# Optimization experiments

Hardware: AMD Instinct MI355X
Metric: run time of the kernel (lower is better)

The kernel has to match this reference:

```python
import jax, jax.numpy as jnp
import numpy as np

B, C, H, W = 8, 256, 32, 32
DK, HEADS = 64, 4
DQ = DK * HEADS            # lambda attention: query dim = dim_key * num_heads
DV = 256 // HEADS          # out_channels // num_heads
EPS = 1e-5
SF = DK ** (-0.25)


def setup_inputs() -> dict:
    key = jax.random.key(0)
    ks = jax.random.split(key, 6)
    inv = 1.0 / np.sqrt(C)
    return {
        "input": jax.random.normal(ks[0], (B, C, H, W), jnp.float32),
        "Wq": jax.random.normal(ks[1], (DQ, C), jnp.float32) * inv,
        "gamma_q": jnp.ones((DQ,), jnp.float32),
        "beta_q": jnp.zeros((DQ,), jnp.float32),
        "Wk": jax.random.normal(ks[2], (DK, C), jnp.float32) * inv,
        "gamma_k": jnp.ones((DK,), jnp.float32),
        "beta_k": jnp.zeros((DK,), jnp.float32),
        "Wv": jax.random.normal(ks[3], (DV, C), jnp.float32) * inv,
        "rpe": jax.random.normal(ks[4], (2 * max(H, W) - 1, 2 * max(H, W) - 1, DK), jnp.float32),
    }


def _bn(x, gamma, beta):
    # BatchNorm2d in training mode: batch stats over (B, H, W), biased variance
    mu = jnp.mean(x, axis=(0, 2, 3), keepdims=True)
    var = jnp.var(x, axis=(0, 2, 3), keepdims=True)
    xn = (x - mu) * jax.lax.rsqrt(var + EPS)
    return xn * gamma[None, :, None, None] + beta[None, :, None, None]


def reference(input, Wq, gamma_q, beta_q, Wk, gamma_k, beta_k, Wv, rpe):
    b, c, h, w = input.shape
    n = h * w
    size = max(h, w)

    # conv1x1 projections (no bias)
    q = _bn(jnp.einsum('oc,bchw->bohw', Wq, input), gamma_q, beta_q)
    k = _bn(jnp.einsum('oc,bchw->bohw', Wk, input), gamma_k, beta_k)
    v = jnp.einsum('oc,bchw->bohw', Wv, input)

    q = q.reshape(b, HEADS, DK, n) * SF          # [b,h,k,n]
    k = k.reshape(b, DK, n) * SF                 # single kv head -> [b,k,n]
    v = v.reshape(b, DV, n)                      # [b,v,n]

    # lambda attention: content lambda
    ks = jax.nn.softmax(k, axis=-1)
    context = jnp.einsum('bkn,bvn->bkv', ks, v)
    out = jnp.einsum('bkv,bhkn->bhvn', context, q)

    # positional lambda via relative position embedding gather
    pos = jnp.arange(size)
    grid = jnp.stack(jnp.meshgrid(pos, pos, indexing='ij'), axis=-1).reshape(-1, 2)  # [n,2]
    rel = grid[None, :] - grid[:, None] + (size - 1)                                 # [n,n,2]
    rg = rpe[rel[..., 0], rel[..., 1]]                                               # [n,n,k]
    pos_context = jnp.einsum('nmk,bvm->bnkv', rg, v)
    out = out + jnp.einsum('bhkn,bnkv->bhvn', q, pos_context)

    return out.reshape(b, -1, h, w)
```

## Files before the change

kernel.cpp:

```cpp
#include <hip/hip_runtime.h>

#define SFC 0.35355339059327373f

typedef __attribute__((ext_vector_type(8))) short short8;
typedef __attribute__((ext_vector_type(16))) float f32x16;
typedef unsigned short ushort_t;

__device__ __forceinline__ float4 ld4(const float* p) { return *reinterpret_cast<const float4*>(p); }
__device__ __forceinline__ void st4(float* p, float4 v) { *reinterpret_cast<float4*>(p) = v; }

union F4 { float4 v; float f[4]; };
union S8 { short8 v; ushort_t u[8]; };

__device__ __forceinline__ ushort_t bfb(float f) {
  union { float f; unsigned u; } a; a.f = f;
  unsigned r = a.u + 0x7FFFu + ((a.u >> 16) & 1u);
  return (ushort_t)(r >> 16);
}
__device__ __forceinline__ float bf2f(ushort_t u) {
  union { unsigned u; float f; } a; a.u = (unsigned)u << 16; return a.f;
}

__device__ __forceinline__ void gl16(const void* g, void* l) {
  __builtin_amdgcn_global_load_lds(
      (const __attribute__((address_space(1))) unsigned int*)g,
      (__attribute__((address_space(3))) unsigned int*)l, 16, 0, 0);
}

__global__ __launch_bounds__(256) void k_prep(
    const float* __restrict__ rpe, const float* __restrict__ wq,
    const float* __restrict__ wk, const float* __restrict__ wv,
    const float* __restrict__ x, ushort_t* __restrict__ RPEB2,
    ushort_t* __restrict__ WB, ushort_t* __restrict__ XBT)
{
  const int bx = blockIdx.x, t = threadIdx.x;
  if (bx < 63) {
    const int di = bx;
#pragma unroll
    for (int it = 0; it < 2; ++it) {
      const int slot = t + it * 256;
      const int tkc = slot >> 6;
      const int l = slot & 63, lnp = l & 31, hip = l >> 5;
      const int dj = (tkc >> 2) * 32 + lnp;
      const int k = (tkc & 3) * 16 + hip * 8;
      S8 o;
      if (dj < 63) {
        const float* s = rpe + (size_t)di * 4032 + dj * 64 + k;
        float4 a = ld4(s), b = ld4(s + 4);
        o.u[0] = bfb(a.x); o.u[1] = bfb(a.y); o.u[2] = bfb(a.z); o.u[3] = bfb(a.w);
        o.u[4] = bfb(b.x); o.u[5] = bfb(b.y); o.u[6] = bfb(b.z); o.u[7] = bfb(b.w);
      } else {
#pragma unroll
        for (int i = 0; i < 8; ++i) o.u[i] = 0;
      }
      *(short8*)(RPEB2 + (size_t)di * 4096 + tkc * 512 + l * 8) = o.v;
    }
  } else if (bx < 111) {
    const int cc = (bx - 63) * 256 + t;
    const int o = cc >> 5, k8 = (cc & 31) * 8;
    const float* src = (o < 256) ? (wq + o * 256)
                      : (o < 320) ? (wk + (o - 256) * 256)
                                  : (wv + (o - 320) * 256);
    float4 a = ld4(src + k8), b = ld4(src + k8 + 4);
    S8 s;
    s.u[0] = bfb(a.x); s.u[1] = bfb(a.y); s.u[2] = bfb(a.z); s.u[3] = bfb(a.w);
    s.u[4] = bfb(b.x); s.u[5] = bfb(b.y); s.u[6] = bfb(b.z); s.u[7] = bfb(b.w);
    *(short8*)(WB + (size_t)o * 256 + k8) = s.v;
  } else {
    const int id = (bx - 111) * 256 + t;
    const int ng = id & 8191, c8 = id >> 13;
    const int bb = ng >> 10, nn = ng & 1023;
    const float* src = x + (size_t)bb * 262144 + (size_t)(c8 * 8) * 1024 + nn;
    S8 s;
#pragma unroll
    for (int j = 0; j < 8; ++j) s.u[j] = bfb(src[(size_t)j * 1024]);
    *(short8*)(XBT + (size_t)ng * 256 + c8 * 8) = s.v;
  }
}

__global__ __launch_bounds__(256) void k_projm(
    const ushort_t* __restrict__ WB, const ushort_t* __restrict__ XBT,
    float* __restrict__ Pk, ushort_t* __restrict__ QB,
    ushort_t* __restrict__ VB2, float* __restrict__ PSUM,
    float* __restrict__ PSQ)
{
  __shared__ ushort_t At[64 * 72];
  __shared__ ushort_t Bt[128 * 72];
  const int t = threadIdx.x;
  const int bm = blockIdx.x, bn = blockIdx.y;
  const int o0 = bm * 64, col0 = bn * 128;
  const int w = t >> 6, l = t & 63, ln = l & 31, hi = l >> 5;
  const int wm = w & 1, wn = w >> 1;

  f32x16 acc0, acc1;
#pragma unroll
  for (int i = 0; i < 16; ++i) { acc0[i] = 0.f; acc1[i] = 0.f; }

  for (int k0 = 0; k0 < 256; k0 += 64) {
    __syncthreads();
#pragma unroll
    for (int i = 0; i < 2; ++i) {
      const int c = t + i * 256, row = c >> 3, k8 = (c & 7) * 8;
      *(short8*)(At + row * 72 + k8) =
          *(const short8*)(WB + (size_t)(o0 + row) * 256 + k0 + k8);
    }
#pragma unroll
    for (int i = 0; i < 4; ++i) {
      const int c = t + i * 256, row = c >> 3, k8 = (c & 7) * 8;
      *(short8*)(Bt + row * 72 + k8) =
          *(const short8*)(XBT + (size_t)(col0 + row) * 256 + k0 + k8);
    }
    __syncthreads();
    const ushort_t* ka  = At + (wm * 32 + ln) * 72 + hi * 8;
    const ushort_t* kb0 = Bt + (wn * 64 + ln) * 72 + hi * 8;
    const ushort_t* kb1 = Bt + (wn * 64 + 32 + ln) * 72 + hi * 8;
#pragma unroll
    for (int kc = 0; kc < 4; ++kc) {
      short8 a = *(const short8*)(ka + kc * 16);
      acc0 = __builtin_amdgcn_mfma_f32_32x32x16_bf16(a, *(const short8*)(kb0 + kc * 16), acc0, 0, 0, 0);
      acc1 = __builtin_amdgcn_mfma_f32_32x32x16_bf16(a, *(const short8*)(kb1 + kc * 16), acc1, 0, 0, 0);
    }
  }

  if (bm == 5) {
    const int b2 = bn >> 3;
    const int n0 = (bn & 7) * 128 + wn * 64 + ln;
#pragma unroll
    for (int r = 0; r < 16; ++r) {
      const int v = wm * 32 + (r & 3) + 8 * (r >> 2) + 4 * hi;
#pragma unroll
      for (int half = 0; half < 2; ++half) {
        const int n = n0 + half * 32;
        const int i2 = n >> 5, j2 = n & 31;
        const float val = half ? acc1[r] : acc0[r];
        VB2[(((size_t)(b2 * 32 + i2) * 2 + wm) * 2 + (j2 >> 4)) * 512
            + ((v & 31) + 32 * ((j2 >> 3) & 1)) * 8 + (j2 & 7)] = bfb(val);
      }
    }
  } else {
    if (bm == 4) {
#pragma unroll
      for (int r = 0; r < 16; ++r) {
        const int o = o0 + wm * 32 + (r & 3) + 8 * (r >> 2) + 4 * hi;
        float* dst = Pk + (size_t)(o - 256) * 8192 + col0 + wn * 64 + ln;
        dst[0]  = acc0[r];
        dst[32] = acc1[r];
      }
    } else {
      const int kcq = 2 * wm;
#pragma unroll
      for (int r = 0; r < 16; ++r) {
        const int kc = kcq + ((r >> 3) & 1);
        const int lq = ln + 32 * ((r >> 2) & 1);
        const int iq = (r & 3) + 4 * hi;
#pragma unroll
        for (int half = 0; half < 2; ++half) {
          const int n = col0 + wn * 64 + half * 32 + ln;
          const int bq_ = n >> 10, i1q = (n >> 5) & 31;
          const float val = half ? acc1[r] : acc0[r];
          QB[(((size_t)(bq_ * 32 + i1q) * 4 + bm) * 4 + kc) * 512 + lq * 8 + iq] =
              bfb(val);
        }
      }
    }
#pragma unroll
    for (int r = 0; r < 16; ++r) {
      float s1 = acc0[r] + acc1[r];
      float s2 = acc0[r] * acc0[r] + acc1[r] * acc1[r];
#pragma unroll
      for (int off = 1; off < 32; off <<= 1) {
        s1 += __shfl_xor(s1, off, 64);
        s2 += __shfl_xor(s2, off, 64);
      }
      if (ln == 0) {
        const int o = o0 + wm * 32 + (r & 3) + 8 * (r >> 2) + 4 * hi;
        PSUM[o * 128 + bn * 2 + wn] = s1;
        PSQ [o * 128 + bn * 2 + wn] = s2;
      }
    }
  }
}

__global__ __launch_bounds__(256) void k_softmax(
    const float* __restrict__ Pk, const float* __restrict__ PSUM,
    const float* __restrict__ PSQ, const float* __restrict__ gq,
    const float* __restrict__ bq, const float* __restrict__ gk,
    const float* __restrict__ bk, float* __restrict__ SCALE,
    float* __restrict__ SHIFT, ushort_t* __restrict__ KSB)
{
  __shared__ float red[8];
  __shared__ float scsh[2];
  const int t = threadIdx.x;

  if (blockIdx.x >= 512) {
    const int ch = blockIdx.x - 512;
    float s1 = 0.f, s2 = 0.f;
    if (t < 128) { s1 = PSUM[ch * 128 + t]; s2 = PSQ[ch * 128 + t]; }
#pragma unroll
    for (int off = 1; off < 64; off <<= 1) {
      s1 += __shfl_xor(s1, off, 64);
      s2 += __shfl_xor(s2, off, 64);
    }
    if ((t & 63) == 0) { red[t >> 6] = s1; red[4 + (t >> 6)] = s2; }
    __syncthreads();
    if (t == 0) {
      s1 = red[0] + red[1] + red[2] + red[3];
      s2 = red[4] + red[5] + red[6] + red[7];
      const float mu = s1 * (1.0f / 8192.0f);
      const float var = s2 * (1.0f / 8192.0f) - mu * mu;
      const float sc = rsqrtf(var + 1e-5f) * gq[ch] * SFC;
      SCALE[ch] = sc;
      SHIFT[ch] = bq[ch] * SFC - mu * sc;
    }
    return;
  }

  const int b = blockIdx.x >> 6, kc = blockIdx.x & 63;
  {
    const int ch = 256 + kc;
    float s1 = 0.f, s2 = 0.f;
    if (t < 128) { s1 = PSUM[ch * 128 + t]; s2 = PSQ[ch * 128 + t]; }
#pragma unroll
    for (int off = 1; off < 64; off <<= 1) {
      s1 += __shfl_xor(s1, off, 64);
      s2 += __shfl_xor(s2, off, 64);
    }
    if ((t & 63) == 0) { red[t >> 6] = s1; red[4 + (t >> 6)] = s2; }
    __syncthreads();
    if (t == 0) {
      s1 = red[0] + red[1] + red[2] + red[3];
      s2 = red[4] + red[5] + red[6] + red[7];
      const float mu = s1 * (1.0f / 8192.0f);
      const float var = s2 * (1.0f / 8192.0f) - mu * mu;
      const float sc = rsqrtf(var + 1e-5f) * gk[kc] * SFC;
      scsh[0] = sc;
      scsh[1] = bk[kc] * SFC - mu * sc;
    }
    __syncthreads();
  }
  const float sc = scsh[0], sh = scsh[1];

  const float4* row = (const float4*)(Pk + (size_t)kc * 8192 + b * 1024);
  float4 v = row[t];
  float y0 = v.x * sc + sh, y1 = v.y * sc + sh;
  float y2 = v.z * sc + sh, y3 = v.w * sc + sh;
  float m = fmaxf(fmaxf(y0, y1), fmaxf(y2, y3));
#pragma unroll
  for (int off = 32; off; off >>= 1) m = fmaxf(m, __shfl_xor(m, off, 64));
  __shared__ float red2[8];
  const int w = t >> 6, lane = t & 63;
  if (lane == 0) red2[w] = m;
  __syncthreads();
  m = fmaxf(fmaxf(red2[0], red2[1]), fmaxf(red2[2], red2[3]));
  const float e0 = __expf(y0 - m), e1 = __expf(y1 - m);
  const float e2 = __expf(y2 - m), e3 = __expf(y3 - m);
  float su = e0 + e1 + e2 + e3;
#pragma unroll
  for (int off = 32; off; off >>= 1) su += __shfl_xor(su, off, 64);
  if (lane == 0) red2[4 + w] = su;
  __syncthreads();
  const float inv = 1.0f / (red2[4] + red2[5] + red2[6] + red2[7]);
  ushort4 u;
  u.x = bfb(e0 * inv); u.y = bfb(e1 * inv);
  u.z = bfb(e2 * inv); u.w = bfb(e3 * inv);
  ((ushort4*)(KSB + (size_t)(b * 64 + kc) * 1024))[t] = u;
}

__global__ __launch_bounds__(256) void k_ctxm(
    const ushort_t* __restrict__ KSB, const ushort_t* __restrict__ VB2,
    ushort_t* __restrict__ CTXB)
{
  __shared__ ushort_t KT[2][64 * 72];
  const int b = blockIdx.x, t = threadIdx.x;
  const int w = t >> 6, l = t & 63, ln = l & 31, hi = l >> 5;
  const int a = w & 1, bt = w >> 1;

  auto stageK = [&](int ch, int buf) {
    const int n0 = ch * 64;
#pragma unroll
    for (int it = 0; it < 2; ++it) {
      const int idx = t + it * 256;
      const int row = idx >> 3, seg = idx & 7;
      *(short8*)(&KT[buf][row * 72 + seg * 8]) =
          *(const short8*)(KSB + (size_t)(b * 64 + row) * 1024 + n0 + seg * 8);
    }
  };

  f32x16 acc;
#pragma unroll
  for (int i = 0; i < 16; ++i) acc[i] = 0.f;

  stageK(0, 0);
  for (int ch = 0; ch < 16; ++ch) {
    const int cur = ch & 1;
    __syncthreads();
    if (ch + 1 < 16) stageK(ch + 1, cur ^ 1);
    const ushort_t* ka = &KT[cur][(a * 32 + ln) * 72 + hi * 8];
#pragma unroll
    for (int cc = 0; cc < 4; ++cc) {
      const int i2 = ch * 2 + (cc >> 1), c = cc & 1;
      short8 bf = *(const short8*)(VB2 +
          (((size_t)(b * 32 + i2) * 2 + bt) * 2 + c) * 512 + l * 8);
      acc = __builtin_amdgcn_mfma_f32_32x32x16_bf16(
          *(const short8*)(ka + cc * 16), bf, acc, 0, 0, 0);
    }
  }
#pragma unroll
  for (int r = 0; r < 16; ++r) {
    const int kc = a * 32 + (r & 3) + 8 * (r >> 2) + 4 * hi;
    CTXB[(size_t)b * 4608 + (bt * 32 + ln) * 72 + kc] = bfb(acc[r]);
  }
}

extern __shared__ char ldsc[];

__global__ __launch_bounds__(512) void k_pos(
    const ushort_t* __restrict__ QB, const ushort_t* __restrict__ RPEB2,
    const ushort_t* __restrict__ VB2, const float* __restrict__ SCALE,
    const float* __restrict__ SHIFT, const ushort_t* __restrict__ CTXB,
    float* __restrict__ out)
{
  float* out_l = (float*)ldsc;
  ushort_t* SlB = (ushort_t*)(ldsc + 33792);
  char* CtxL = ldsc + 54272;

  const int t = threadIdx.x;
  const int b = blockIdx.x >> 5, i1 = blockIdx.x & 31;
  const int w = t >> 6, l = t & 63, ln = l & 31, hi = l >> 5;
  const int m = w & 3, g = w >> 2;

  {
    const char* cs = (const char*)CTXB + (size_t)b * 9216;
    gl16(cs + w * 1024 + l * 16, CtxL + w * 1024 + l * 16);
    if (w == 0) gl16(cs + 8192 + l * 16, CtxL + 8192 + l * 16);
  }

  const ushort_t* rbase = RPEB2 + (size_t)(g * 16 - i1 + 31) * 4096;
  const ushort_t* vbase = VB2 + (size_t)(b * 32 + g * 16) * 2048;

  short8 rA[8], rB[8];
#pragma unroll
  for (int f = 0; f < 8; ++f) rA[f] = *(const short8*)(rbase + f * 512 + l * 8);

  short8 qf[4];
  {
    const ushort_t* qb = QB + (((size_t)(b * 32 + i1) * 4 + m) * 4) * 512 + l * 8;
#pragma unroll
    for (int kc = 0; kc < 4; ++kc) {
      S8 raw; raw.v = *(const short8*)(qb + kc * 512);
      const int chb = m * 64 + kc * 16 + hi * 8;
      F4 s0, s1, h0, h1;
      s0.v = ld4(SCALE + chb); s1.v = ld4(SCALE + chb + 4);
      h0.v = ld4(SHIFT + chb); h1.v = ld4(SHIFT + chb + 4);
      S8 o;
#pragma unroll
      for (int i = 0; i < 8; ++i) {
        const float f = bf2f(raw.u[i]);
        const float scv = (i < 4) ? s0.f[i] : s1.f[i - 4];
        const float shv = (i < 4) ? h0.f[i] : h1.f[i - 4];
        o.u[i] = bfb(f * scv + shv);
      }
      qf[kc] = o.v;
    }
  }

  f32x16 sv0, sv1;
#pragma unroll
  for (int i = 0; i < 16; ++i) { sv0[i] = 0.f; sv1[i] = 0.f; }

  ushort_t* sm = SlB + w * 1280;

  auto body = [&](int s, const short8* R) {
    const ushort_t* vp = vbase + (size_t)s * 2048 + l * 8;
    short8 v00 = *(const short8*)(vp);
    short8 v01 = *(const short8*)(vp + 512);
    short8 v10 = *(const short8*)(vp + 1024);
    short8 v11 = *(const short8*)(vp + 1536);
    f32x16 t0, t1;
#pragma unroll
    for (int i = 0; i < 16; ++i) { t0[i] = 0.f; t1[i] = 0.f; }
#pragma unroll
    for (int kc = 0; kc < 4; ++kc) {
      t0 = __builtin_amdgcn_mfma_f32_32x32x16_bf16(qf[kc], R[kc],     t0, 0, 0, 0);
      t1 = __builtin_amdgcn_mfma_f32_32x32x16_bf16(qf[kc], R[4 + kc], t1, 0, 0, 0);
    }
#pragma unroll
    for (int r = 0; r < 16; ++r) {
      const int j1 = (r & 3) + 8 * (r >> 2) + 4 * hi;
      const int j2a = ln + j1 - 31;
      const int j2b = 32 + ln + j1 - 31;
      if ((unsigned)j2a < 32u) sm[j1 * 40 + j2a] = bfb(t0[r]);
      if ((unsigned)j2b < 32u) sm[j1 * 40 + j2b] = bfb(t1[r]);
    }
    const ushort_t* sa = sm + ln * 40 + hi * 8;
    short8 sA0 = *(const short8*)(sa);
    short8 sA1 = *(const short8*)(sa + 16);
    sv0 = __builtin_amdgcn_mfma_f32_32x32x16_bf16(sA0, v00, sv0, 0, 0, 0);
    sv0 = __builtin_amdgcn_mfma_f32_32x32x16_bf16(sA1, v01, sv0, 0, 0, 0);
    sv1 = __builtin_amdgcn_mfma_f32_32x32x16_bf16(sA0, v10, sv1, 0, 0, 0);
    sv1 = __builtin_amdgcn_mfma_f32_32x32x16_bf16(sA1, v11, sv1, 0, 0, 0);
  };

  for (int s = 0; s < 16; s += 2) {
    {
      const ushort_t* rn = rbase + (size_t)(s + 1) * 4096;
#pragma unroll
      for (int f = 0; f < 8; ++f) rB[f] = *(const short8*)(rn + f * 512 + l * 8);
    }
    body(s, rA);
    if (s + 2 < 16) {
      const ushort_t* rn = rbase + (size_t)(s + 2) * 4096;
#pragma unroll
      for (int f = 0; f < 8; ++f) rA[f] = *(const short8*)(rn + f * 512 + l * 8);
    }
    body(s + 1, rB);
  }

  __syncthreads();

  if (g == 0) {
    const ushort_t* cb = (const ushort_t*)CtxL;
    const ushort_t* c0 = cb + ln * 72 + hi * 8;
    const ushort_t* c1 = cb + (32 + ln) * 72 + hi * 8;
#pragma unroll
    for (int kc = 0; kc < 4; ++kc) {
      sv0 = __builtin_amdgcn_mfma_f32_32x32x16_bf16(qf[kc], *(const short8*)(c0 + kc * 16), sv0, 0, 0, 0);
      sv1 = __builtin_amdgcn_mfma_f32_32x32x16_bf16(qf[kc], *(const short8*)(c1 + kc * 16), sv1, 0, 0, 0);
    }
  } else {
#pragma unroll
    for (int r = 0; r < 16; ++r) {
      const int j1 = (r & 3) + 8 * (r >> 2) + 4 * hi;
      out_l[(m * 64 + ln) * 33 + j1]      = sv0[r];
      out_l[(m * 64 + 32 + ln) * 33 + j1] = sv1[r];
    }
  }
  __syncthreads();
  if (g == 0) {
#pragma unroll
    for (int r = 0; r < 16; ++r) {
      const int j1 = (r & 3) + 8 * (r >> 2) + 4 * hi;
      out_l[(m * 64 + ln) * 33 + j1]      += sv0[r];
      out_l[(m * 64 + 32 + ln) * 33 + j1] += sv1[r];
    }
  }
  __syncthreads();
  {
    const int ch = t >> 1, jh = (t & 1) * 16;
    float* dst = out + (size_t)b * 262144 + (size_t)ch * 1024 + i1 * 32 + jh;
    const float* srow = out_l + ch * 33 + jh;
#pragma unroll
    for (int gq2 = 0; gq2 < 4; ++gq2)
      st4(dst + gq2 * 4, make_float4(srow[gq2 * 4], srow[gq2 * 4 + 1],
                                     srow[gq2 * 4 + 2], srow[gq2 * 4 + 3]));
  }
}

extern "C" void kernel_launch(void* const* d_in, const int* in_sizes, int n_in,
                              void* d_out, int out_size, void* d_ws, size_t ws_size,
                              hipStream_t stream) {
  const float* x   = (const float*)d_in[0];
  const float* wq  = (const float*)d_in[1];
  const float* gq  = (const float*)d_in[2];
  const float* bq  = (const float*)d_in[3];
  const float* wk  = (const float*)d_in[4];
  const float* gk  = (const float*)d_in[5];
  const float* bk  = (const float*)d_in[6];
  const float* wv  = (const float*)d_in[7];
  const float* rpe = (const float*)d_in[8];
  float* out = (float*)d_out;
  char* W = (char*)d_ws;

  float* Pk       = (float*)W;
  ushort_t* QB    = (ushort_t*)(W + 2097152);
  ushort_t* KSB   = (ushort_t*)(W + 6291456);
  float* PSUM     = (float*)(W + 7340032);
  float* PSQ      = (float*)(W + 7503872);
  float* SCALE    = (float*)(W + 7667712);
  float* SHIFT    = (float*)(W + 7669760);
  ushort_t* CTXB  = (ushort_t*)(W + 7671808);
  ushort_t* RPEB2 = (ushort_t*)(W + 7745536);
  ushort_t* VB2   = (ushort_t*)(W + 8261632);
  ushort_t* WB    = (ushort_t*)(W + 9310208);
  ushort_t* XBT   = (ushort_t*)(W + 9506816);

  k_prep<<<1135, 256, 0, stream>>>(rpe, wq, wk, wv, x, RPEB2, WB, XBT);
  k_projm<<<dim3(6, 64), 256, 0, stream>>>(WB, XBT, Pk, QB, VB2, PSUM, PSQ);
  k_softmax<<<768, 256, 0, stream>>>(Pk, PSUM, PSQ, gq, bq, gk, bk, SCALE, SHIFT, KSB);
  k_ctxm<<<8, 256, 0, stream>>>(KSB, VB2, CTXB);

  hipFuncSetAttribute((const void*)k_pos,
                      hipFuncAttributeMaxDynamicSharedMemorySize, 63488);
  k_pos<<<256, 512, 63488, stream>>>(QB, RPEB2, VB2, SCALE, SHIFT, CTXB, out);
}
```

Baseline: 59.41 us.

## Fuse key softmax with context reduction and drop separate MFMA context kernel

```diff
diff --git a/kernel.cpp b/kernel.cpp
--- a/kernel.cpp
+++ b/kernel.cpp
@@ -181,15 +181,17 @@
   }
 }
 
-__global__ __launch_bounds__(256) void k_softmax(
+__global__ __launch_bounds__(256) void k_softctx(
     const float* __restrict__ Pk, const float* __restrict__ PSUM,
     const float* __restrict__ PSQ, const float* __restrict__ gq,
     const float* __restrict__ bq, const float* __restrict__ gk,
     const float* __restrict__ bk, float* __restrict__ SCALE,
-    float* __restrict__ SHIFT, ushort_t* __restrict__ KSB)
+    float* __restrict__ SHIFT, const ushort_t* __restrict__ VB2,
+    ushort_t* __restrict__ CTXB)
 {
   __shared__ float red[8];
   __shared__ float scsh[2];
+  __shared__ float cpart[4][64];
   const int t = threadIdx.x;
 
   if (blockIdx.x >= 512) {
@@ -240,16 +242,16 @@
   }
   const float sc = scsh[0], sh = scsh[1];
 
-  const float4* row = (const float4*)(Pk + (size_t)kc * 8192 + b * 1024);
-  float4 v = row[t];
-  float y0 = v.x * sc + sh, y1 = v.y * sc + sh;
-  float y2 = v.z * sc + sh, y3 = v.w * sc + sh;
+  const float4* rowp = (const float4*)(Pk + (size_t)kc * 8192 + b * 1024);
+  float4 pv = rowp[t];
+  float y0 = pv.x * sc + sh, y1 = pv.y * sc + sh;
+  float y2 = pv.z * sc + sh, y3 = pv.w * sc + sh;
   float m = fmaxf(fmaxf(y0, y1), fmaxf(y2, y3));
 #pragma unroll
   for (int off = 32; off; off >>= 1) m = fmaxf(m, __shfl_xor(m, off, 64));
   __shared__ float red2[8];
-  const int w = t >> 6, lane = t & 63;
-  if (lane == 0) red2[w] = m;
+  const int w = t >> 6, l = t & 63;
+  if (l == 0) red2[w] = m;
   __syncthreads();
   m = fmaxf(fmaxf(red2[0], red2[1]), fmaxf(red2[2], red2[3]));
   const float e0 = __expf(y0 - m), e1 = __expf(y1 - m);
@@ -257,58 +259,72 @@
   float su = e0 + e1 + e2 + e3;
 #pragma unroll
   for (int off = 32; off; off >>= 1) su += __shfl_xor(su, off, 64);
-  if (lane == 0) red2[4 + w] = su;
+  if (l == 0) red2[4 + w] = su;
   __syncthreads();
   const float inv = 1.0f / (red2[4] + red2[5] + red2[6] + red2[7]);
-  ushort4 u;
-  u.x = bfb(e0 * inv); u.y = bfb(e1 * inv);
-  u.z = bfb(e2 * inv); u.w = bfb(e3 * inv);
-  ((ushort4*)(KSB + (size_t)(b * 64 + kc) * 1024))[t] = u;
-}
-
-__global__ __launch_bounds__(256) void k_ctxm(
-    const ushort_t* __restrict__ KSB, const ushort_t* __restrict__ VB2,
-    ushort_t* __restrict__ CTXB)
-{
-  __shared__ ushort_t KT[2][64 * 72];
-  const int b = blockIdx.x, t = threadIdx.x;
-  const int w = t >> 6, l = t & 63, ln = l & 31, hi = l >> 5;
-  const int a = w & 1, bt = w >> 1;
-
-  auto stageK = [&](int ch, int buf) {
-    const int n0 = ch * 64;
-#pragma unroll
-    for (int it = 0; it < 2; ++it) {
-      const int idx = t + it * 256;
-      const int row = idx >> 3, seg = idx & 7;
-      *(short8*)(&KT[buf][row * 72 + seg * 8]) =
-          *(const short8*)(KSB + (size_t)(b * 64 + row) * 1024 + n0 + seg * 8);
-    }
-  };
-
-  f32x16 acc;
-#pragma unroll
-  for (int i = 0; i < 16; ++i) acc[i] = 0.f;
-
-  stageK(0, 0);
-  for (int ch = 0; ch < 16; ++ch) {
-    const int cur = ch & 1;
-    __syncthreads();
-    if (ch + 1 < 16) stageK(ch + 1, cur ^ 1);
-    const ushort_t* ka = &KT[cur][(a * 32 + ln) * 72 + hi * 8];
-#pragma unroll
-    for (int cc = 0; cc < 4; ++cc) {
-      const int i2 = ch * 2 + (cc >> 1), c = cc & 1;
-      short8 bf = *(const short8*)(VB2 +
-          (((size_t)(b * 32 + i2) * 2 + bt) * 2 + c) * 512 + l * 8);
-      acc = __builtin_amdgcn_mfma_f32_32x32x16_bf16(
-          *(const short8*)(ka + cc * 16), bf, acc, 0, 0, 0);
-    }
-  }
-#pragma unroll
-  for (int r = 0; r < 16; ++r) {
-    const int kc = a * 32 + (r & 3) + 8 * (r >> 2) + 4 * hi;
-    CTXB[(size_t)b * 4608 + (bt * 32 + ln) * 72 + kc] = bfb(acc[r]);
+  const float k0v = e0 * inv, k1v = e1 * inv, k2v = e2 * inv, k3v = e3 * inv;
+
+  const int n0 = t * 4;
+  const int i2 = n0 >> 5;
+  const int cX = (n0 >> 4) & 1, hi2 = (n0 >> 3) & 1, i0 = n0 & 7;
+  const ushort_t* vbL = VB2 + (((size_t)(b * 32 + i2) * 2 + 0) * 2 + cX) * 512
+                        + (32 * hi2) * 8 + i0;
+  const ushort_t* vbH = vbL + 1024;
+  float a64[64];
+#pragma unroll
+  for (int v = 0; v < 32; ++v) {
+    ushort4 u = *(const ushort4*)(vbL + v * 8);
+    a64[v] = k0v * bf2f(u.x) + k1v * bf2f(u.y) + k2v * bf2f(u.z) + k3v * bf2f(u.w);
+  }
+#pragma unroll
+  for (int v = 0; v < 32; ++v) {
+    ushort4 u = *(const ushort4*)(vbH + v * 8);
+    a64[32 + v] = k0v * bf2f(u.x) + k1v * bf2f(u.y) + k2v * bf2f(u.z) + k3v * bf2f(u.w);
+  }
+  float c32[32];
+#pragma unroll
+  for (int j = 0; j < 32; ++j) {
+    const float mine = (l & 32) ? a64[j + 32] : a64[j];
+    const float send = (l & 32) ? a64[j] : a64[j + 32];
+    c32[j] = mine + __shfl_xor(send, 32, 64);
+  }
+  float c16[16];
+#pragma unroll
+  for (int j = 0; j < 16; ++j) {
+    const float mine = (l & 16) ? c32[j + 16] : c32[j];
+    const float send = (l & 16) ? c32[j] : c32[j + 16];
+    c16[j] = mine + __shfl_xor(send, 16, 64);
+  }
+  float c8[8];
+#pragma unroll
+  for (int j = 0; j < 8; ++j) {
+    const float mine = (l & 8) ? c16[j + 8] : c16[j];
+    const float send = (l & 8) ? c16[j] : c16[j + 8];
+    c8[j] = mine + __shfl_xor(send, 8, 64);
+  }
+  float c4[4];
+#pragma unroll
+  for (int j = 0; j < 4; ++j) {
+    const float mine = (l & 4) ? c8[j + 4] : c8[j];
+    const float send = (l & 4) ? c8[j] : c8[j + 4];
+    c4[j] = mine + __shfl_xor(send, 4, 64);
+  }
+  float c2[2];
+#pragma unroll
+  for (int j = 0; j < 2; ++j) {
+    const float mine = (l & 2) ? c4[j + 2] : c4[j];
+    const float send = (l & 2) ? c4[j] : c4[j + 2];
+    c2[j] = mine + __shfl_xor(send, 2, 64);
+  }
+  {
+    const float mine = (l & 1) ? c2[1] : c2[0];
+    const float send = (l & 1) ? c2[0] : c2[1];
+    cpart[w][l] = mine + __shfl_xor(send, 1, 64);
+  }
+  __syncthreads();
+  if (w == 0) {
+    const float s = cpart[0][l] + cpart[1][l] + cpart[2][l] + cpart[3][l];
+    CTXB[(size_t)b * 4608 + l * 72 + kc] = bfb(s);
   }
 }
 
@@ -473,21 +489,20 @@
 
   float* Pk       = (float*)W;
   ushort_t* QB    = (ushort_t*)(W + 2097152);
-  ushort_t* KSB   = (ushort_t*)(W + 6291456);
-  float* PSUM     = (float*)(W + 7340032);
-  float* PSQ      = (float*)(W + 7503872);
-  float* SCALE    = (float*)(W + 7667712);
-  float* SHIFT    = (float*)(W + 7669760);
-  ushort_t* CTXB  = (ushort_t*)(W + 7671808);
-  ushort_t* RPEB2 = (ushort_t*)(W + 7745536);
-  ushort_t* VB2   = (ushort_t*)(W + 8261632);
-  ushort_t* WB    = (ushort_t*)(W + 9310208);
-  ushort_t* XBT   = (ushort_t*)(W + 9506816);
+  float* PSUM     = (float*)(W + 6291456);
+  float* PSQ      = (float*)(W + 6455296);
+  float* SCALE    = (float*)(W + 6619136);
+  float* SHIFT    = (float*)(W + 6621184);
+  ushort_t* CTXB  = (ushort_t*)(W + 6623232);
+  ushort_t* RPEB2 = (ushort_t*)(W + 6696960);
+  ushort_t* VB2   = (ushort_t*)(W + 7213056);
+  ushort_t* WB    = (ushort_t*)(W + 8261632);
+  ushort_t* XBT   = (ushort_t*)(W + 8458240);
 
   k_prep<<<1135, 256, 0, stream>>>(rpe, wq, wk, wv, x, RPEB2, WB, XBT);
   k_projm<<<dim3(6, 64), 256, 0, stream>>>(WB, XBT, Pk, QB, VB2, PSUM, PSQ);
-  k_softmax<<<768, 256, 0, stream>>>(Pk, PSUM, PSQ, gq, bq, gk, bk, SCALE, SHIFT, KSB);
-  k_ctxm<<<8, 256, 0, stream>>>(KSB, VB2, CTXB);
+  k_softctx<<<768, 256, 0, stream>>>(Pk, PSUM, PSQ, gq, bq, gk, bk,
+                                     SCALE, SHIFT, VB2, CTXB);
 
   hipFuncSetAttribute((const void*)k_pos,
                       hipFuncAttributeMaxDynamicSharedMemorySize, 63488);
```

Result: no change. 59.69 us (+0.5%).
